# Kernel tuning notes

Measured on AMD Instinct MI355X. Metric: run time of the kernel, lower is better.

## Reference

```python
import jax, jax.numpy as jnp
from jax import lax
import numpy as np
import math

D = 256; H = 4; DH = 64; PERIOD = 30; WIN = 4; L = 2
AUDIO = 768; MOTION = 33
B = 8; T = 1024; S = 1024


def _pe_table(t, d=D, period=PERIOD):
    pos = np.arange(period, dtype=np.float32)[:, None]
    div = np.exp(np.arange(0, d, 2, dtype=np.float32) * (-math.log(10000.0) / d))
    pe = np.zeros((period, d), np.float32)
    pe[:, 0::2] = np.sin(pos * div)
    pe[:, 1::2] = np.cos(pos * div)
    reps = t // period + 1
    return jnp.asarray(np.tile(pe, (reps, 1))[:t])


def _tgt_mask(t):
    # ALiBi-style bias (quantized by period) + causal mask, per head. [H,t,t]
    slopes = jnp.array([0.25 ** (i + 1) for i in range(H)], jnp.float32)
    i = jnp.arange(t)[:, None]
    j = jnp.arange(t)[None, :]
    rel = i - j
    alibi = jnp.where(rel >= 0, -(rel // PERIOD).astype(jnp.float32), 0.0)
    causal = jnp.where(rel >= 0, 0.0, -jnp.inf)
    return slopes[:, None, None] * alibi + causal[None]


def _mem_mask(t, s):
    i = jnp.arange(t)[:, None]
    j = jnp.arange(s)[None, :]
    return jnp.where(jnp.abs(i - j) <= WIN, 0.0, -jnp.inf)


def _ln(x, g, b, eps=1e-5):
    mu = jnp.mean(x, -1, keepdims=True)
    var = jnp.mean(jnp.square(x - mu), -1, keepdims=True)
    return (x - mu) * lax.rsqrt(var + eps) * g + b


def _mha(xq, xkv, in_w, in_b, out_w, out_b, mask):
    wq, wk, wv = jnp.split(in_w, 3, axis=0)
    bq, bk, bv = jnp.split(in_b, 3)
    q = xq @ wq.T + bq
    k = xkv @ wk.T + bk
    v = xkv @ wv.T + bv
    b_, t_, _ = q.shape
    s_ = k.shape[1]
    q = q.reshape(b_, t_, H, DH)
    k = k.reshape(b_, s_, H, DH)
    v = v.reshape(b_, s_, H, DH)
    scores = jnp.einsum('bthd,bshd->bhts', q, k) / math.sqrt(DH) + mask
    a = jax.nn.softmax(scores, axis=-1)
    o = jnp.einsum('bhts,bshd->bthd', a, v).reshape(b_, t_, D)
    return o @ out_w.T + out_b


def _conv1d(x_nch, w, b):
    y = lax.conv_general_dilated(x_nch, w, (1,), [(2, 2)],
                                 dimension_numbers=('NCH', 'OIH', 'NCH'))
    return y + b[None, :, None]


def setup_inputs() -> dict:
    key = jax.random.key(0)
    ks = iter(jax.random.split(key, 40))

    def r(shape, s=0.05):
        return jax.random.normal(next(ks), shape, jnp.float32) * s

    return {
        'hidden_states': jax.random.normal(next(ks), (B, S, AUDIO), jnp.float32),
        'target_motions': jax.random.uniform(next(ks), (B, T, MOTION), jnp.float32),
        'W_af': r((D, AUDIO)), 'b_af': r((D,)),
        'conv1_w': r((D, D, 5)), 'conv1_b': r((D,)),
        'conv2_w': r((D, D, 5)), 'conv2_b': r((D,)),
        'W_vm': r((D, MOTION)), 'b_vm': r((D,)),
        'sa_in_w': r((L, 3 * D, D)), 'sa_in_b': r((L, 3 * D)),
        'sa_out_w': r((L, D, D)), 'sa_out_b': r((L, D)),
        'ca_in_w': r((L, 3 * D, D)), 'ca_in_b': r((L, 3 * D)),
        'ca_out_w': r((L, D, D)), 'ca_out_b': r((L, D)),
        'ln1_g': jnp.ones((L, D)), 'ln1_b': jnp.zeros((L, D)),
        'ln2_g': jnp.ones((L, D)), 'ln2_b': jnp.zeros((L, D)),
        'ln3_g': jnp.ones((L, D)), 'ln3_b': jnp.zeros((L, D)),
        'ff1_w': r((L, 2 * D, D)), 'ff1_b': r((L, 2 * D)),
        'ff2_w': r((L, D, 2 * D)), 'ff2_b': r((L, D)),
        'W_vr': r((MOTION, D)), 'b_vr': r((MOTION,)),
    }


def reference(hidden_states, target_motions, W_af, b_af, conv1_w, conv1_b,
              conv2_w, conv2_b, W_vm, b_vm, sa_in_w, sa_in_b, sa_out_w,
              sa_out_b, ca_in_w, ca_in_b, ca_out_w, ca_out_b, ln1_g, ln1_b,
              ln2_g, ln2_b, ln3_g, ln3_b, ff1_w, ff1_b, ff2_w, ff2_b,
              W_vr, b_vr):
    # audio encoder: linear + residual temporal convs (exact GELU)
    audio = hidden_states @ W_af.T + b_af                       # [B,S,D]
    c = _conv1d(audio.transpose(0, 2, 1), conv1_w, conv1_b)
    c = jax.nn.gelu(c, approximate=False)
    c = _conv1d(c, conv2_w, conv2_b)
    audio = audio + c.transpose(0, 2, 1)

    b_, t_, _ = target_motions.shape
    motion_in = jnp.concatenate(
        [jnp.zeros((b_, 1, MOTION), target_motions.dtype),
         target_motions[:, :-1]], axis=1)
    x = motion_in @ W_vm.T + b_vm + _pe_table(t_)               # PPE (eval: no dropout)

    tm = _tgt_mask(t_)                                          # [H,t,t]
    mm = _mem_mask(t_, audio.shape[1])                          # [t,s]

    for l in range(L):  # post-norm TransformerDecoderLayer, relu FFN
        x = _ln(x + _mha(x, x, sa_in_w[l], sa_in_b[l], sa_out_w[l], sa_out_b[l], tm),
                ln1_g[l], ln1_b[l])
        x = _ln(x + _mha(x, audio, ca_in_w[l], ca_in_b[l], ca_out_w[l], ca_out_b[l], mm),
                ln2_g[l], ln2_b[l])
        h = jax.nn.relu(x @ ff1_w[l].T + ff1_b[l]) @ ff2_w[l].T + ff2_b[l]
        x = _ln(x + h, ln3_g[l], ln3_b[l])

    return jnp.clip(x @ W_vr.T + b_vr, 0.0, 1.0)
```

## Files before the change

### kernel.cpp

```cpp
#include <hip/hip_runtime.h>
#include <math.h>

#define B_ 8
#define T_ 1024
#define S_ 1024
#define D_ 256
#define H_ 4
#define DH_ 64
#define AUDIO_ 768
#define MOTION_ 33
#define PERIOD_ 30
#define WIN_ 4
#define M_ (B_ * T_)

typedef _Float16 half8 __attribute__((ext_vector_type(8)));
typedef _Float16 half4 __attribute__((ext_vector_type(4)));
typedef __attribute__((ext_vector_type(4))) float f32x4;

#define O_AF    0
#define O_SAIN  196608
#define O_SAOUT 589824
#define O_CAIN  720896
#define O_CAOUT 1114112
#define O_FF1   1245184
#define O_FF2   1507328
#define O_CONV1 1769472
#define O_CONV2 2097152
#define O_VR    2424832
#define WH_TOT  2441216
#define HID_TOT 6291456

struct CvtSrc { const float* p[17]; };

__global__ __launch_bounds__(256) void cvt_all(
    CvtSrc s, _Float16* __restrict__ wH, _Float16* __restrict__ hidH) {
  const long i = (long)blockIdx.x * 256 + threadIdx.x;
  if (i >= (long)WH_TOT + HID_TOT) return;
  if (i >= WH_TOT) { const long j = i - WH_TOT; hidH[j] = (_Float16)s.p[15][j]; return; }
  if (i >= O_VR) {
    const long j = i - O_VR, oc = j >> 8, cin = j & 255;
    wH[i] = (oc < MOTION_) ? (_Float16)s.p[16][oc * 256 + cin] : (_Float16)0.f;
    return;
  }
  if (i >= O_CONV2) {
    const long j = i - O_CONV2, oc = j / 1280, r = j % 1280, tap = r >> 8, cin = r & 255;
    wH[i] = (_Float16)s.p[14][(oc * 256 + cin) * 5 + tap]; return;
  }
  if (i >= O_CONV1) {
    const long j = i - O_CONV1, oc = j / 1280, r = j % 1280, tap = r >> 8, cin = r & 255;
    wH[i] = (_Float16)s.p[13][(oc * 256 + cin) * 5 + tap]; return;
  }
  int seg; long base;
  if      (i >= 1638400) { seg = 12; base = 1638400; }
  else if (i >= 1507328) { seg = 11; base = 1507328; }
  else if (i >= 1376256) { seg = 10; base = 1376256; }
  else if (i >= 1245184) { seg = 9;  base = 1245184; }
  else if (i >= 1179648) { seg = 8;  base = 1179648; }
  else if (i >= 1114112) { seg = 7;  base = 1114112; }
  else if (i >= 917504)  { seg = 6;  base = 917504; }
  else if (i >= 720896)  { seg = 5;  base = 720896; }
  else if (i >= 655360)  { seg = 4;  base = 655360; }
  else if (i >= 589824)  { seg = 3;  base = 589824; }
  else if (i >= 393216)  { seg = 2;  base = 393216; }
  else if (i >= 196608)  { seg = 1;  base = 196608; }
  else                   { seg = 0;  base = 0; }
  wH[i] = (_Float16)s.p[seg][i - base];
}

__global__ __launch_bounds__(256) void gemm_h(
    const _Float16* __restrict__ A, const _Float16* __restrict__ W,
    const float* __restrict__ bias, float* __restrict__ Cf,
    _Float16* __restrict__ Ch, int M, int N, int K, int relu) {
  __shared__ _Float16 As[2][64][72];
  __shared__ _Float16 Bs[2][64][72];
  const int tid = threadIdx.x;
  const int wave = tid >> 6, lane = tid & 63;
  const int wr = wave >> 1, wc = wave & 1;
  const int lr16 = lane & 15, kq = lane >> 4;
  const int bm = blockIdx.x, bn = blockIdx.y;
  const int sr = tid >> 2, sq = tid & 3;

  const _Float16* Ap = A + (size_t)(bm * 64 + sr) * K + sq * 8;
  const _Float16* Wp = W + (size_t)(bn * 64 + sr) * K + sq * 8;

  half8 ra0 = *reinterpret_cast<const half8*>(Ap);
  half8 ra1 = *reinterpret_cast<const half8*>(Ap + 32);
  half8 rw0 = *reinterpret_cast<const half8*>(Wp);
  half8 rw1 = *reinterpret_cast<const half8*>(Wp + 32);
  f32x4 acc[2][2] = {};

  *reinterpret_cast<half8*>(&As[0][sr][sq * 8]) = ra0;
  *reinterpret_cast<half8*>(&As[0][sr][32 + sq * 8]) = ra1;
  *reinterpret_cast<half8*>(&Bs[0][sr][sq * 8]) = rw0;
  *reinterpret_cast<half8*>(&Bs[0][sr][32 + sq * 8]) = rw1;
  __syncthreads();

  const int nsteps = K >> 6;
  for (int step = 0; step < nsteps; ++step) {
    const int cur = step & 1;
    const bool more = (step + 1 < nsteps);
    if (more) {
      const int kn = (step + 1) << 6;
      ra0 = *reinterpret_cast<const half8*>(Ap + kn);
      ra1 = *reinterpret_cast<const half8*>(Ap + kn + 32);
      rw0 = *reinterpret_cast<const half8*>(Wp + kn);
      rw1 = *reinterpret_cast<const half8*>(Wp + kn + 32);
    }
    half8 af[2][2], bf[2][2];
#pragma unroll
    for (int m = 0; m < 2; ++m)
#pragma unroll
      for (int s = 0; s < 2; ++s)
        af[m][s] = *reinterpret_cast<const half8*>(
            &As[cur][wr * 32 + m * 16 + lr16][s * 32 + kq * 8]);
#pragma unroll
    for (int n = 0; n < 2; ++n)
#pragma unroll
      for (int s = 0; s < 2; ++s)
        bf[n][s] = *reinterpret_cast<const half8*>(
            &Bs[cur][wc * 32 + n * 16 + lr16][s * 32 + kq * 8]);
#pragma unroll
    for (int m = 0; m < 2; ++m)
#pragma unroll
      for (int n = 0; n < 2; ++n)
#pragma unroll
        for (int s = 0; s < 2; ++s)
          acc[m][n] = __builtin_amdgcn_mfma_f32_16x16x32_f16(af[m][s], bf[n][s], acc[m][n], 0, 0, 0);
    if (more) {
      *reinterpret_cast<half8*>(&As[cur ^ 1][sr][sq * 8]) = ra0;
      *reinterpret_cast<half8*>(&As[cur ^ 1][sr][32 + sq * 8]) = ra1;
      *reinterpret_cast<half8*>(&Bs[cur ^ 1][sr][sq * 8]) = rw0;
      *reinterpret_cast<half8*>(&Bs[cur ^ 1][sr][32 + sq * 8]) = rw1;
      __syncthreads();
    }
  }

#pragma unroll
  for (int m = 0; m < 2; ++m) {
#pragma unroll
    for (int n = 0; n < 2; ++n) {
      const int col = bn * 64 + wc * 32 + n * 16 + lr16;
      const float bv = bias[col];
#pragma unroll
      for (int j = 0; j < 4; ++j) {
        const int row = bm * 64 + wr * 32 + m * 16 + kq * 4 + j;
        float v = acc[m][n][j] + bv;
        if (relu) v = fmaxf(v, 0.f);
        const size_t idx = (size_t)row * N + col;
        if (Cf) Cf[idx] = v;
        if (Ch) Ch[idx] = (_Float16)v;
      }
    }
  }
}

__global__ __launch_bounds__(256) void gemm_ca(
    const _Float16* __restrict__ Aq, const _Float16* __restrict__ Akv,
    const _Float16* __restrict__ W, const float* __restrict__ bias,
    _Float16* __restrict__ Oq, _Float16* __restrict__ Okv) {
  __shared__ _Float16 As[2][64][72];
  __shared__ _Float16 Bs[2][64][72];
  const int tid = threadIdx.x;
  const int wave = tid >> 6, lane = tid & 63;
  const int wr = wave >> 1, wc = wave & 1;
  const int lr16 = lane & 15, kq = lane >> 4;
  const int bm = blockIdx.x, bn = blockIdx.y;
  const int sr = tid >> 2, sq = tid & 3;
  const bool isq = (bn < 4);
  const _Float16* A = isq ? Aq : Akv;
  _Float16* Optr = isq ? Oq : Okv;
  const int Nout = isq ? 256 : 512;
  const int ocol0 = (isq ? bn : bn - 4) * 64;

  const _Float16* Ap = A + (size_t)(bm * 64 + sr) * 256 + sq * 8;
  const _Float16* Wp = W + (size_t)(bn * 64 + sr) * 256 + sq * 8;

  half8 ra0 = *reinterpret_cast<const half8*>(Ap);
  half8 ra1 = *reinterpret_cast<const half8*>(Ap + 32);
  half8 rw0 = *reinterpret_cast<const half8*>(Wp);
  half8 rw1 = *reinterpret_cast<const half8*>(Wp + 32);
  f32x4 acc[2][2] = {};

  *reinterpret_cast<half8*>(&As[0][sr][sq * 8]) = ra0;
  *reinterpret_cast<half8*>(&As[0][sr][32 + sq * 8]) = ra1;
  *reinterpret_cast<half8*>(&Bs[0][sr][sq * 8]) = rw0;
  *reinterpret_cast<half8*>(&Bs[0][sr][32 + sq * 8]) = rw1;
  __syncthreads();

  for (int step = 0; step < 4; ++step) {
    const int cur = step & 1;
    const bool more = (step + 1 < 4);
    if (more) {
      const int kn = (step + 1) << 6;
      ra0 = *reinterpret_cast<const half8*>(Ap + kn);
      ra1 = *reinterpret_cast<const half8*>(Ap + kn + 32);
      rw0 = *reinterpret_cast<const half8*>(Wp + kn);
      rw1 = *reinterpret_cast<const half8*>(Wp + kn + 32);
    }
    half8 af[2][2], bf[2][2];
#pragma unroll
    for (int m = 0; m < 2; ++m)
#pragma unroll
      for (int s = 0; s < 2; ++s)
        af[m][s] = *reinterpret_cast<const half8*>(
            &As[cur][wr * 32 + m * 16 + lr16][s * 32 + kq * 8]);
#pragma unroll
    for (int n = 0; n < 2; ++n)
#pragma unroll
      for (int s = 0; s < 2; ++s)
        bf[n][s] = *reinterpret_cast<const half8*>(
            &Bs[cur][wc * 32 + n * 16 + lr16][s * 32 + kq * 8]);
#pragma unroll
    for (int m = 0; m < 2; ++m)
#pragma unroll
      for (int n = 0; n < 2; ++n)
#pragma unroll
        for (int s = 0; s < 2; ++s)
          acc[m][n] = __builtin_amdgcn_mfma_f32_16x16x32_f16(af[m][s], bf[n][s], acc[m][n], 0, 0, 0);
    if (more) {
      *reinterpret_cast<half8*>(&As[cur ^ 1][sr][sq * 8]) = ra0;
      *reinterpret_cast<half8*>(&As[cur ^ 1][sr][32 + sq * 8]) = ra1;
      *reinterpret_cast<half8*>(&Bs[cur ^ 1][sr][sq * 8]) = rw0;
      *reinterpret_cast<half8*>(&Bs[cur ^ 1][sr][32 + sq * 8]) = rw1;
      __syncthreads();
    }
  }

#pragma unroll
  for (int m = 0; m < 2; ++m) {
#pragma unroll
    for (int n = 0; n < 2; ++n) {
      const int lc = wc * 32 + n * 16 + lr16;
      const float bv = bias[bn * 64 + lc];
#pragma unroll
      for (int j = 0; j < 4; ++j) {
        const int row = bm * 64 + wr * 32 + m * 16 + kq * 4 + j;
        Optr[(size_t)row * Nout + ocol0 + lc] = (_Float16)(acc[m][n][j] + bv);
      }
    }
  }
}

__device__ __forceinline__ half8 conv_ld(const _Float16* Xb, int p, int tap, int cin) {
  const int sp = p + tap - 2;
  if (sp < 0 || sp >= S_) { half8 z = {}; return z; }
  return *reinterpret_cast<const half8*>(Xb + (size_t)sp * D_ + cin);
}

__global__ __launch_bounds__(256) void conv_h(
    const _Float16* __restrict__ Xh, const _Float16* __restrict__ Wc,
    const float* __restrict__ bias, _Float16* OutH,
    const _Float16* ResH, int mode) {
  __shared__ _Float16 As[2][64][72];
  __shared__ _Float16 Bs[2][64][72];
  const int tid = threadIdx.x;
  const int wave = tid >> 6, lane = tid & 63;
  const int wr = wave >> 1, wc = wave & 1;
  const int lr16 = lane & 15, kq = lane >> 4;
  const int b = blockIdx.x >> 4;
  const int s0 = (blockIdx.x & 15) * 64;
  const int o0 = blockIdx.y * 64;
  const int sr = tid >> 2, sq = tid & 3;

  const _Float16* Xb = Xh + (size_t)b * S_ * D_;
  const _Float16* Wp = Wc + (size_t)(o0 + sr) * 1280 + sq * 8;
  const int p = s0 + sr;

  half8 ra0 = conv_ld(Xb, p, 0, sq * 8);
  half8 ra1 = conv_ld(Xb, p, 0, 32 + sq * 8);
  half8 rw0 = *reinterpret_cast<const half8*>(Wp);
  half8 rw1 = *reinterpret_cast<const half8*>(Wp + 32);
  f32x4 acc[2][2] = {};

  *reinterpret_cast<half8*>(&As[0][sr][sq * 8]) = ra0;
  *reinterpret_cast<half8*>(&As[0][sr][32 + sq * 8]) = ra1;
  *reinterpret_cast<half8*>(&Bs[0][sr][sq * 8]) = rw0;
  *reinterpret_cast<half8*>(&Bs[0][sr][32 + sq * 8]) = rw1;
  __syncthreads();

  for (int step = 0; step < 20; ++step) {
    const int cur = step & 1;
    const bool more = (step + 1 < 20);
    if (more) {
      const int kn = (step + 1) << 6;
      const int tap = kn >> 8, cb = kn & 255;
      ra0 = conv_ld(Xb, p, tap, cb + sq * 8);
      ra1 = conv_ld(Xb, p, tap, cb + 32 + sq * 8);
      rw0 = *reinterpret_cast<const half8*>(Wp + kn);
      rw1 = *reinterpret_cast<const half8*>(Wp + kn + 32);
    }
    half8 af[2][2], bf[2][2];
#pragma unroll
    for (int m = 0; m < 2; ++m)
#pragma unroll
      for (int s = 0; s < 2; ++s)
        af[m][s] = *reinterpret_cast<const half8*>(
            &As[cur][wr * 32 + m * 16 + lr16][s * 32 + kq * 8]);
#pragma unroll
    for (int n = 0; n < 2; ++n)
#pragma unroll
      for (int s = 0; s < 2; ++s)
        bf[n][s] = *reinterpret_cast<const half8*>(
            &Bs[cur][wc * 32 + n * 16 + lr16][s * 32 + kq * 8]);
#pragma unroll
    for (int m = 0; m < 2; ++m)
#pragma unroll
      for (int n = 0; n < 2; ++n)
#pragma unroll
        for (int s = 0; s < 2; ++s)
          acc[m][n] = __builtin_amdgcn_mfma_f32_16x16x32_f16(af[m][s], bf[n][s], acc[m][n], 0, 0, 0);
    if (more) {
      *reinterpret_cast<half8*>(&As[cur ^ 1][sr][sq * 8]) = ra0;
      *reinterpret_cast<half8*>(&As[cur ^ 1][sr][32 + sq * 8]) = ra1;
      *reinterpret_cast<half8*>(&Bs[cur ^ 1][sr][sq * 8]) = rw0;
      *reinterpret_cast<half8*>(&Bs[cur ^ 1][sr][32 + sq * 8]) = rw1;
      __syncthreads();
    }
  }

#pragma unroll
  for (int m = 0; m < 2; ++m) {
#pragma unroll
    for (int n = 0; n < 2; ++n) {
      const int oc = o0 + wc * 32 + n * 16 + lr16;
      const float bv = bias[oc];
#pragma unroll
      for (int j = 0; j < 4; ++j) {
        const int s = s0 + wr * 32 + m * 16 + kq * 4 + j;
        const size_t idx = ((size_t)b * S_ + s) * D_ + oc;
        float v = acc[m][n][j] + bv;
        if (mode == 0) {
          v = 0.5f * v * (1.f + erff(v * 0.70710678118654752f));
        } else {
          v += (float)ResH[idx];
        }
        OutH[idx] = (_Float16)v;
      }
    }
  }
}

__global__ __launch_bounds__(256) void head_mfma(
    const _Float16* __restrict__ Xh, const _Float16* __restrict__ Wh,
    const float* __restrict__ bv, float* __restrict__ Out) {
  __shared__ _Float16 As[2][64][72];
  __shared__ _Float16 Bs[2][64][72];
  const int tid = threadIdx.x;
  const int wave = tid >> 6, lane = tid & 63;
  const int wr = wave >> 1, wc = wave & 1;
  const int lr16 = lane & 15, kq = lane >> 4;
  const int bm = blockIdx.x;
  const int sr = tid >> 2, sq = tid & 3;

  const _Float16* Ap = Xh + (size_t)(bm * 64 + sr) * D_ + sq * 8;
  const _Float16* Wp = Wh + (size_t)sr * D_ + sq * 8;

  half8 ra0 = *reinterpret_cast<const half8*>(Ap);
  half8 ra1 = *reinterpret_cast<const half8*>(Ap + 32);
  half8 rw0 = *reinterpret_cast<const half8*>(Wp);
  half8 rw1 = *reinterpret_cast<const half8*>(Wp + 32);
  f32x4 acc[2][2] = {};

  *reinterpret_cast<half8*>(&As[0][sr][sq * 8]) = ra0;
  *reinterpret_cast<half8*>(&As[0][sr][32 + sq * 8]) = ra1;
  *reinterpret_cast<half8*>(&Bs[0][sr][sq * 8]) = rw0;
  *reinterpret_cast<half8*>(&Bs[0][sr][32 + sq * 8]) = rw1;
  __syncthreads();

  for (int step = 0; step < 4; ++step) {
    const int cur = step & 1;
    const bool more = (step + 1 < 4);
    if (more) {
      const int kn = (step + 1) << 6;
      ra0 = *reinterpret_cast<const half8*>(Ap + kn);
      ra1 = *reinterpret_cast<const half8*>(Ap + kn + 32);
      rw0 = *reinterpret_cast<const half8*>(Wp + kn);
      rw1 = *reinterpret_cast<const half8*>(Wp + kn + 32);
    }
    half8 af[2][2], bf[2][2];
#pragma unroll
    for (int m = 0; m < 2; ++m)
#pragma unroll
      for (int s = 0; s < 2; ++s)
        af[m][s] = *reinterpret_cast<const half8*>(
            &As[cur][wr * 32 + m * 16 + lr16][s * 32 + kq * 8]);
#pragma unroll
    for (int n = 0; n < 2; ++n)
#pragma unroll
      for (int s = 0; s < 2; ++s)
        bf[n][s] = *reinterpret_cast<const half8*>(
            &Bs[cur][wc * 32 + n * 16 + lr16][s * 32 + kq * 8]);
#pragma unroll
    for (int m = 0; m < 2; ++m)
#pragma unroll
      for (int n = 0; n < 2; ++n)
#pragma unroll
        for (int s = 0; s < 2; ++s)
          acc[m][n] = __builtin_amdgcn_mfma_f32_16x16x32_f16(af[m][s], bf[n][s], acc[m][n], 0, 0, 0);
    if (more) {
      *reinterpret_cast<half8*>(&As[cur ^ 1][sr][sq * 8]) = ra0;
      *reinterpret_cast<half8*>(&As[cur ^ 1][sr][32 + sq * 8]) = ra1;
      *reinterpret_cast<half8*>(&Bs[cur ^ 1][sr][sq * 8]) = rw0;
      *reinterpret_cast<half8*>(&Bs[cur ^ 1][sr][32 + sq * 8]) = rw1;
      __syncthreads();
    }
  }

#pragma unroll
  for (int m = 0; m < 2; ++m) {
#pragma unroll
    for (int n = 0; n < 2; ++n) {
      const int col = wc * 32 + n * 16 + lr16;
      if (col < MOTION_) {
        const float bb = bv[col];
#pragma unroll
        for (int j = 0; j < 4; ++j) {
          const int row = bm * 64 + wr * 32 + m * 16 + kq * 4 + j;
          float v = acc[m][n][j] + bb;
          Out[(size_t)row * MOTION_ + col] = fminf(fmaxf(v, 0.f), 1.f);
        }
      }
    }
  }
}

__global__ __launch_bounds__(256) void motion_pe(
    const float* __restrict__ TM, const float* __restrict__ Wvm,
    const float* __restrict__ bvm, float* __restrict__ Xout,
    _Float16* __restrict__ XoutH) {
  const int d = threadIdx.x;
  const int bt = blockIdx.x;
  const int t = bt & (T_ - 1);
  const int b = bt >> 10;
  float acc = bvm[d];
  if (t > 0) {
    const float* mrow = TM + ((size_t)b * T_ + t - 1) * MOTION_;
    const float* wrow = Wvm + (size_t)d * MOTION_;
#pragma unroll
    for (int m = 0; m < MOTION_; ++m) acc += mrow[m] * wrow[m];
  }
  const int pos = t % PERIOD_;
  const int i2 = d >> 1;
  const float div = expf((float)(2 * i2) * (-9.210340371976184f / 256.f));
  const float ang = (float)pos * div;
  acc += (d & 1) ? cosf(ang) : sinf(ang);
  Xout[(size_t)bt * D_ + d] = acc;
  XoutH[(size_t)bt * D_ + d] = (_Float16)acc;
}

#define RSK_ 72
#define RSV_ 64
__global__ __launch_bounds__(512) void self_attn(
    const _Float16* __restrict__ QKV, _Float16* __restrict__ O) {
  __shared__ _Float16 Ks[2][64 * RSK_];
  __shared__ _Float16 VTs[2][64 * RSV_];
  __shared__ _Float16 Ps[8][16 * RSK_];
  const int qtb = blockIdx.x, h = blockIdx.y, b = blockIdx.z;
  const int tid = threadIdx.x;
  const int wave = tid >> 6, lane = tid & 63;
  const int lo = lane & 15, hi = lane >> 4;
  const float slope = exp2f(-2.f * (float)(h + 1));
  const int qloc = wave * 16 + lo;
  const int tq = qtb * 128 + qloc;
  const size_t base = (size_t)b * T_ * 768 + h * 64;
  const int sj = tid >> 3, sch = tid & 7;

  half8 qf[2];
#pragma unroll
  for (int s = 0; s < 2; ++s)
    qf[s] = *reinterpret_cast<const half8*>(
        QKV + base + (size_t)(qtb * 128 + qloc) * 768 + s * 32 + hi * 8);

  f32x4 oacc[4] = {};
  float mrun = -1e30f, lrun = 0.f;

  const int nkt = 2 * qtb + 2;

  half8 rk, rv;
  {
    const size_t rowoff = base + (size_t)sj * 768;
    rk = *reinterpret_cast<const half8*>(QKV + rowoff + 256 + sch * 8);
    rv = *reinterpret_cast<const half8*>(QKV + rowoff + 512 + sch * 8);
    *reinterpret_cast<half8*>(&Ks[0][sj * RSK_ + sch * 8]) = rk;
#pragma unroll
    for (int r = 0; r < 8; ++r) {
      const int d = sch * 8 + r;
      const int sw = ((d & 7) ^ (d >> 3)) << 3;
      VTs[0][d * RSV_ + (sj ^ sw)] = rv[r];
    }
  }
  __syncthreads();

  for (int kt = 0; kt < nkt; ++kt) {
    const int cur = kt & 1;
    const bool more = (kt + 1 < nkt);
    if (more) {
      const size_t rowoff = base + (size_t)((kt + 1) * 64 + sj) * 768;
      rk = *reinterpret_cast<const half8*>(QKV + rowoff + 256 + sch * 8);
      rv = *reinterpret_cast<const half8*>(QKV + rowoff + 512 + sch * 8);
    }

    f32x4 st[4] = {};
    __builtin_amdgcn_s_setprio(1);
#pragma unroll
    for (int f = 0; f < 4; ++f) {
#pragma unroll
      for (int s = 0; s < 2; ++s) {
        const half8 kf = *reinterpret_cast<const half8*>(
            &Ks[cur][(f * 16 + lo) * RSK_ + s * 32 + hi * 8]);
        st[f] = __builtin_amdgcn_mfma_f32_16x16x32_f16(kf, qf[s], st[f], 0, 0, 0);
      }
    }
    __builtin_amdgcn_s_setprio(0);

    float sc[4][4];
    float tmax = -1e30f;
#pragma unroll
    for (int f = 0; f < 4; ++f)
#pragma unroll
      for (int r = 0; r < 4; ++r) {
        const int j = kt * 64 + f * 16 + hi * 4 + r;
        const int rel = tq - j;
        const float v = (rel >= 0)
            ? st[f][r] * 0.125f - slope * (float)(rel / PERIOD_) : -1e30f;
        sc[f][r] = v;
        tmax = fmaxf(tmax, v);
      }
    tmax = fmaxf(tmax, __shfl_xor(tmax, 16, 64));
    tmax = fmaxf(tmax, __shfl_xor(tmax, 32, 64));
    const float mnew = fmaxf(mrun, tmax);
    const float scale = __expf(mrun - mnew);

    float psum = 0.f;
#pragma unroll
    for (int f = 0; f < 4; ++f) {
      half4 ph;
#pragma unroll
      for (int r = 0; r < 4; ++r) {
        const float pv = __expf(sc[f][r] - mnew);
        psum += pv;
        ph[r] = (_Float16)pv;
      }
      *reinterpret_cast<half4*>(&Ps[wave][lo * RSK_ + f * 16 + hi * 4]) = ph;
    }
    psum += __shfl_xor(psum, 16, 64);
    psum += __shfl_xor(psum, 32, 64);
    lrun = lrun * scale + psum;
    mrun = mnew;

    float rsc[4];
#pragma unroll
    for (int r = 0; r < 4; ++r) rsc[r] = __shfl(scale, hi * 4 + r, 64);
#pragma unroll
    for (int nf = 0; nf < 4; ++nf)
#pragma unroll
      for (int r = 0; r < 4; ++r) oacc[nf][r] *= rsc[r];

    __builtin_amdgcn_s_setprio(1);
#pragma unroll
    for (int s = 0; s < 2; ++s) {
      const half8 pf = *reinterpret_cast<const half8*>(
          &Ps[wave][lo * RSK_ + s * 32 + hi * 8]);
#pragma unroll
      for (int nf = 0; nf < 4; ++nf) {
        const int d = nf * 16 + lo;
        const int sw = ((d & 7) ^ (d >> 3)) << 3;
        const half8 vf = *reinterpret_cast<const half8*>(
            &VTs[cur][d * RSV_ + ((s * 32 + hi * 8) ^ sw)]);
        oacc[nf] = __builtin_amdgcn_mfma_f32_16x16x32_f16(pf, vf, oacc[nf], 0, 0, 0);
      }
    }
    __builtin_amdgcn_s_setprio(0);

    if (more) {
      *reinterpret_cast<half8*>(&Ks[cur ^ 1][sj * RSK_ + sch * 8]) = rk;
#pragma unroll
      for (int r = 0; r < 8; ++r) {
        const int d = sch * 8 + r;
        const int sw = ((d & 7) ^ (d >> 3)) << 3;
        VTs[cur ^ 1][d * RSV_ + (sj ^ sw)] = rv[r];
      }
      __syncthreads();
    }
  }

  float invl[4];
#pragma unroll
  for (int r = 0; r < 4; ++r) invl[r] = 1.f / __shfl(lrun, hi * 4 + r, 64);
#pragma unroll
  for (int nf = 0; nf < 4; ++nf)
#pragma unroll
    for (int r = 0; r < 4; ++r) {
      const int q = qtb * 128 + wave * 16 + hi * 4 + r;
      O[((size_t)b * T_ + q) * D_ + h * 64 + nf * 16 + lo] =
          (_Float16)(oacc[nf][r] * invl[r]);
    }
}

__global__ __launch_bounds__(128) void cross_attn(
    const _Float16* __restrict__ Q, const _Float16* __restrict__ KV,
    _Float16* __restrict__ O) {
  const int gid = blockIdx.x * 128 + threadIdx.x;
  const int h = gid & 3;
  const int bt = gid >> 2;
  const int t = bt & (T_ - 1);
  const int b = bt >> 10;

  float q[64];
  const _Float16* qp = Q + (size_t)bt * D_ + h * 64;
#pragma unroll
  for (int d0 = 0; d0 < 64; d0 += 8) {
    const half8 v = *reinterpret_cast<const half8*>(qp + d0);
#pragma unroll
    for (int e = 0; e < 8; ++e) q[d0 + e] = (float)v[e];
  }

  const int j0 = (t - WIN_ > 0) ? t - WIN_ : 0;
  const int j1 = (t + WIN_ < S_ - 1) ? t + WIN_ : S_ - 1;
  const int nj = j1 - j0 + 1;

  float sc[9];
  float mx = -1e30f;
#pragma unroll
  for (int jj = 0; jj < 9; ++jj) {
    if (jj < nj) {
      const _Float16* kp = KV + ((size_t)b * S_ + j0 + jj) * 512 + h * 64;
      float s = 0.f;
#pragma unroll
      for (int d0 = 0; d0 < 64; d0 += 8) {
        const half8 kv = *reinterpret_cast<const half8*>(kp + d0);
#pragma unroll
        for (int e = 0; e < 8; ++e) s += q[d0 + e] * (float)kv[e];
      }
      sc[jj] = s * 0.125f;
      mx = fmaxf(mx, sc[jj]);
    } else {
      sc[jj] = -1e30f;
    }
  }
  float l = 0.f;
  float p[9];
#pragma unroll
  for (int jj = 0; jj < 9; ++jj) { p[jj] = __expf(sc[jj] - mx); l += p[jj]; }
  const float inv = 1.f / l;

  float o[64];
#pragma unroll
  for (int d = 0; d < 64; ++d) o[d] = 0.f;
#pragma unroll
  for (int jj = 0; jj < 9; ++jj) {
    if (jj < nj) {
      const float pj = p[jj] * inv;
      const _Float16* vp = KV + ((size_t)b * S_ + j0 + jj) * 512 + 256 + h * 64;
#pragma unroll
      for (int d0 = 0; d0 < 64; d0 += 8) {
        const half8 vv = *reinterpret_cast<const half8*>(vp + d0);
#pragma unroll
        for (int e = 0; e < 8; ++e) o[d0 + e] += pj * (float)vv[e];
      }
    }
  }
  _Float16* op = O + (size_t)bt * D_ + h * 64;
#pragma unroll
  for (int d = 0; d < 64; ++d) op[d] = (_Float16)o[d];
}

__global__ __launch_bounds__(256) void ln_res(
    const float* X, const _Float16* __restrict__ R,
    const float* __restrict__ g, const float* __restrict__ bta,
    float* Out, _Float16* __restrict__ OutH) {
  const int wid = threadIdx.x >> 6, lane = threadIdx.x & 63;
  const size_t row = (size_t)blockIdx.x * 4 + wid;
  const float* xp = X + row * D_;
  const _Float16* rp = R + row * D_;
  float v[4];
  float s = 0.f;
#pragma unroll
  for (int k = 0; k < 4; ++k) {
    const int d = lane + k * 64;
    v[k] = xp[d] + (float)rp[d];
    s += v[k];
  }
#pragma unroll
  for (int off = 32; off; off >>= 1) s += __shfl_xor(s, off, 64);
  const float mu = s * (1.f / 256.f);
  float var = 0.f;
#pragma unroll
  for (int k = 0; k < 4; ++k) { const float d = v[k] - mu; var += d * d; }
#pragma unroll
  for (int off = 32; off; off >>= 1) var += __shfl_xor(var, off, 64);
  const float rs = rsqrtf(var * (1.f / 256.f) + 1e-5f);
#pragma unroll
  for (int k = 0; k < 4; ++k) {
    const int d = lane + k * 64;
    const float o = (v[k] - mu) * rs * g[d] + bta[d];
    Out[row * D_ + d] = o;
    OutH[row * D_ + d] = (_Float16)o;
  }
}

extern "C" void kernel_launch(void* const* d_in, const int* in_sizes, int n_in,
                              void* d_out, int out_size, void* d_ws, size_t ws_size,
                              hipStream_t stream) {
  (void)in_sizes; (void)n_in; (void)out_size; (void)ws_size;
  const float* hidden = (const float*)d_in[0];
  const float* tmot   = (const float*)d_in[1];
  const float* W_af   = (const float*)d_in[2];
  const float* b_af   = (const float*)d_in[3];
  const float* c1w    = (const float*)d_in[4];
  const float* c1b    = (const float*)d_in[5];
  const float* c2w    = (const float*)d_in[6];
  const float* c2b    = (const float*)d_in[7];
  const float* Wvm    = (const float*)d_in[8];
  const float* bvm    = (const float*)d_in[9];
  const float* sa_in_w  = (const float*)d_in[10];
  const float* sa_in_b  = (const float*)d_in[11];
  const float* sa_out_w = (const float*)d_in[12];
  const float* sa_out_b = (const float*)d_in[13];
  const float* ca_in_w  = (const float*)d_in[14];
  const float* ca_in_b  = (const float*)d_in[15];
  const float* ca_out_w = (const float*)d_in[16];
  const float* ca_out_b = (const float*)d_in[17];
  const float* ln1g = (const float*)d_in[18];
  const float* ln1b = (const float*)d_in[19];
  const float* ln2g = (const float*)d_in[20];
  const float* ln2b = (const float*)d_in[21];
  const float* ln3g = (const float*)d_in[22];
  const float* ln3b = (const float*)d_in[23];
  const float* ff1w = (const float*)d_in[24];
  const float* ff1b = (const float*)d_in[25];
  const float* ff2w = (const float*)d_in[26];
  const float* ff2b = (const float*)d_in[27];
  const float* Wvr  = (const float*)d_in[28];
  const float* bvr  = (const float*)d_in[29];
  float* out = (float*)d_out;

  float* ws = (float*)d_ws;
  const size_t BSD = (size_t)M_ * D_;
  float* x     = ws + BSD;
  _Float16* t1h = (_Float16*)(ws + 2 * BSD);
  _Float16* hb = (_Float16*)(ws + 3 * BSD);
  _Float16* Rh      = hb;
  _Float16* x_h     = hb + 3 * BSD;
  _Float16* audio_h = hb + 4 * BSD;
  _Float16* att_h   = hb + 5 * BSD;
  _Float16* wH      = hb + 6 * BSD;
  _Float16* ckv_h   = Rh + BSD;

  const dim3 blk(256);

  CvtSrc cs;
  cs.p[0] = W_af;
  cs.p[1] = sa_in_w;            cs.p[2] = sa_in_w + 768 * 256;
  cs.p[3] = sa_out_w;           cs.p[4] = sa_out_w + 256 * 256;
  cs.p[5] = ca_in_w;            cs.p[6] = ca_in_w + 768 * 256;
  cs.p[7] = ca_out_w;           cs.p[8] = ca_out_w + 256 * 256;
  cs.p[9] = ff1w;               cs.p[10] = ff1w + 512 * 256;
  cs.p[11] = ff2w;              cs.p[12] = ff2w + 256 * 512;
  cs.p[13] = c1w;               cs.p[14] = c2w;
  cs.p[15] = hidden;            cs.p[16] = Wvr;
  cvt_all<<<dim3((WH_TOT + HID_TOT + 255) / 256), blk, 0, stream>>>(cs, wH, Rh);

  gemm_h<<<dim3(M_ / 64, 4), blk, 0, stream>>>(Rh, wH + O_AF, b_af, nullptr, audio_h,
                                               M_, 256, 768, 0);
  conv_h<<<dim3(128, 4), blk, 0, stream>>>(audio_h, wH + O_CONV1, c1b, t1h, nullptr, 0);
  conv_h<<<dim3(128, 4), blk, 0, stream>>>(t1h, wH + O_CONV2, c2b, audio_h, audio_h, 1);

  motion_pe<<<dim3(M_), blk, 0, stream>>>(tmot, Wvm, bvm, x, x_h);

  for (int l = 0; l < 2; ++l) {
    gemm_h<<<dim3(M_ / 64, 12), blk, 0, stream>>>(
        x_h, wH + O_SAIN + l * 196608, sa_in_b + l * 768, nullptr, Rh, M_, 768, 256, 0);
    self_attn<<<dim3(T_ / 128, H_, B_), dim3(512), 0, stream>>>(Rh, att_h);
    gemm_h<<<dim3(M_ / 64, 4), blk, 0, stream>>>(
        att_h, wH + O_SAOUT + l * 65536, sa_out_b + l * 256, nullptr, t1h, M_, 256, 256, 0);
    ln_res<<<dim3(M_ / 4), blk, 0, stream>>>(x, t1h, ln1g + l * 256, ln1b + l * 256, x, x_h);

    gemm_ca<<<dim3(M_ / 64, 12), blk, 0, stream>>>(
        x_h, audio_h, wH + O_CAIN + l * 196608, ca_in_b + l * 768, Rh, ckv_h);
    cross_attn<<<dim3(M_ * H_ / 128), dim3(128), 0, stream>>>(Rh, ckv_h, att_h);
    gemm_h<<<dim3(M_ / 64, 4), blk, 0, stream>>>(
        att_h, wH + O_CAOUT + l * 65536, ca_out_b + l * 256, nullptr, t1h, M_, 256, 256, 0);
    ln_res<<<dim3(M_ / 4), blk, 0, stream>>>(x, t1h, ln2g + l * 256, ln2b + l * 256, x, x_h);

    gemm_h<<<dim3(M_ / 64, 8), blk, 0, stream>>>(
        x_h, wH + O_FF1 + l * 131072, ff1b + l * 512, nullptr, Rh, M_, 512, 256, 1);
    gemm_h<<<dim3(M_ / 64, 4), blk, 0, stream>>>(
        Rh, wH + O_FF2 + l * 131072, ff2b + l * 256, nullptr, t1h, M_, 256, 512, 0);
    ln_res<<<dim3(M_ / 4), blk, 0, stream>>>(x, t1h, ln3g + l * 256, ln3b + l * 256, x, x_h);
  }

  head_mfma<<<dim3(M_ / 64), blk, 0, stream>>>(x_h, wH + O_VR, bvr, out);
}
```

Before: 336.4 us.

## Split causal self-attention KV range across two blocks and merge partials

```diff
diff --git a/kernel.cpp b/kernel.cpp
--- a/kernel.cpp
+++ b/kernel.cpp
@@ -12,6 +12,7 @@
 #define PERIOD_ 30
 #define WIN_ 4
 #define M_ (B_ * T_)
+#define PART_ (B_ * H_ * T_)
 
 typedef _Float16 half8 __attribute__((ext_vector_type(8)));
 typedef _Float16 half4 __attribute__((ext_vector_type(4)));
@@ -451,11 +452,13 @@
 #define RSK_ 72
 #define RSV_ 64
 __global__ __launch_bounds__(512) void self_attn(
-    const _Float16* __restrict__ QKV, _Float16* __restrict__ O) {
+    const _Float16* __restrict__ QKV, float* __restrict__ Opart,
+    float* __restrict__ Ml, float* __restrict__ Ll) {
   __shared__ _Float16 Ks[2][64 * RSK_];
   __shared__ _Float16 VTs[2][64 * RSV_];
   __shared__ _Float16 Ps[8][16 * RSK_];
-  const int qtb = blockIdx.x, h = blockIdx.y, b = blockIdx.z;
+  const int qtb = blockIdx.x >> 1, half = blockIdx.x & 1;
+  const int h = blockIdx.y, b = blockIdx.z;
   const int tid = threadIdx.x;
   const int wave = tid >> 6, lane = tid & 63;
   const int lo = lane & 15, hi = lane >> 4;
@@ -474,11 +477,12 @@
   f32x4 oacc[4] = {};
   float mrun = -1e30f, lrun = 0.f;
 
-  const int nkt = 2 * qtb + 2;
+  const int nloc = qtb + 1;
+  const int kt0 = half * nloc;
 
   half8 rk, rv;
   {
-    const size_t rowoff = base + (size_t)sj * 768;
+    const size_t rowoff = base + (size_t)(kt0 * 64 + sj) * 768;
     rk = *reinterpret_cast<const half8*>(QKV + rowoff + 256 + sch * 8);
     rv = *reinterpret_cast<const half8*>(QKV + rowoff + 512 + sch * 8);
     *reinterpret_cast<half8*>(&Ks[0][sj * RSK_ + sch * 8]) = rk;
@@ -491,9 +495,10 @@
   }
   __syncthreads();
 
-  for (int kt = 0; kt < nkt; ++kt) {
-    const int cur = kt & 1;
-    const bool more = (kt + 1 < nkt);
+  for (int i = 0; i < nloc; ++i) {
+    const int kt = kt0 + i;
+    const int cur = i & 1;
+    const bool more = (i + 1 < nloc);
     if (more) {
       const size_t rowoff = base + (size_t)((kt + 1) * 64 + sj) * 768;
       rk = *reinterpret_cast<const half8*>(QKV + rowoff + 256 + sch * 8);
@@ -528,7 +533,7 @@
       }
     tmax = fmaxf(tmax, __shfl_xor(tmax, 16, 64));
     tmax = fmaxf(tmax, __shfl_xor(tmax, 32, 64));
-    const float mnew = fmaxf(mrun, tmax);
+    const float mnew = fmaxf(fmaxf(mrun, tmax), -1e20f);
     const float scale = __expf(mrun - mnew);
 
     float psum = 0.f;
@@ -584,17 +589,39 @@
     }
   }
 
-  float invl[4];
-#pragma unroll
-  for (int r = 0; r < 4; ++r) invl[r] = 1.f / __shfl(lrun, hi * 4 + r, 64);
+  const size_t rbase = ((size_t)b * H_ + h) * T_;
+  const size_t hoff = (size_t)half * PART_;
 #pragma unroll
   for (int nf = 0; nf < 4; ++nf)
 #pragma unroll
     for (int r = 0; r < 4; ++r) {
       const int q = qtb * 128 + wave * 16 + hi * 4 + r;
-      O[((size_t)b * T_ + q) * D_ + h * 64 + nf * 16 + lo] =
-          (_Float16)(oacc[nf][r] * invl[r]);
-    }
+      Opart[(hoff + rbase + q) * 64 + nf * 16 + lo] = oacc[nf][r];
+    }
+  if (hi == 0) {
+    const int q = qtb * 128 + wave * 16 + lo;
+    Ml[hoff + rbase + q] = mrun;
+    Ll[hoff + rbase + q] = lrun;
+  }
+}
+
+__global__ __launch_bounds__(256) void attn_merge(
+    const float* __restrict__ Opart, const float* __restrict__ Ml,
+    const float* __restrict__ Ll, _Float16* __restrict__ O) {
+  const int tid = threadIdx.x;
+  const int d = tid & 63;
+  const long row = (long)blockIdx.x * 4 + (tid >> 6);
+  const float m0 = Ml[row], m1 = Ml[PART_ + row];
+  const float l0 = Ll[row], l1 = Ll[PART_ + row];
+  const float m = fmaxf(m0, m1);
+  const float w0 = __expf(m0 - m), w1 = __expf(m1 - m);
+  const float inv = 1.f / (l0 * w0 + l1 * w1);
+  const float o = (Opart[row * 64 + d] * w0 +
+                   Opart[(long)PART_ * 64 + row * 64 + d] * w1) * inv;
+  const int b = (int)(row >> 12);
+  const int h = (int)((row >> 10) & 3);
+  const int t = (int)(row & (T_ - 1));
+  O[(((size_t)b * T_ + t) * D_) + h * 64 + d] = (_Float16)o;
 }
 
 __global__ __launch_bounds__(128) void cross_attn(
@@ -746,6 +773,9 @@
   _Float16* att_h   = hb + 5 * BSD;
   _Float16* wH      = hb + 6 * BSD;
   _Float16* ckv_h   = Rh + BSD;
+  float* Opart = (float*)(wH + WH_TOT);
+  float* Ml    = Opart + (size_t)2 * PART_ * 64;
+  float* Ll    = Ml + (size_t)2 * PART_;
 
   const dim3 blk(256);
 
@@ -771,7 +801,8 @@
   for (int l = 0; l < 2; ++l) {
     gemm_h<<<dim3(M_ / 64, 12), blk, 0, stream>>>(
         x_h, wH + O_SAIN + l * 196608, sa_in_b + l * 768, nullptr, Rh, M_, 768, 256, 0);
-    self_attn<<<dim3(T_ / 128, H_, B_), dim3(512), 0, stream>>>(Rh, att_h);
+    self_attn<<<dim3(T_ / 128 * 2, H_, B_), dim3(512), 0, stream>>>(Rh, Opart, Ml, Ll);
+    attn_merge<<<dim3(PART_ / 4), blk, 0, stream>>>(Opart, Ml, Ll, att_h);
     gemm_h<<<dim3(M_ / 64, 4), blk, 0, stream>>>(
         att_h, wH + O_SAOUT + l * 65536, sa_out_b + l * 256, nullptr, t1h, M_, 256, 256, 0);
     ln_res<<<dim3(M_ / 4), blk, 0, stream>>>(x, t1h, ln1g + l * 256, ln1b + l * 256, x, x_h);
```

Measured after the change: 332.9 us. Within noise of the previous version (-1.0%).
